# Kernel tuning notes

Measured on AMD Instinct MI355X. Metric: run time of the kernel, lower is better.

Reference implementation:

```python
import jax, jax.numpy as jnp
import numpy as np

N = 100000      # nodes
E = 1600000     # edges
G = 64          # graphs in batch
H = 128         # hidden (== num_features)
L = 4           # num_layers
C = 16          # num_classes
NCAND = 100000  # candidate edges
BN_EPS = 1e-5


def setup_inputs() -> dict:
    key = jax.random.key(0)
    ks = jax.random.split(key, 24)
    s = 0.05
    inp = {}
    inp["x"] = jax.random.normal(ks[0], (N, H), dtype=jnp.float32)
    inp["edge_index"] = jax.random.randint(ks[1], (2, E), 0, N)
    inp["batch"] = jnp.sort(jax.random.randint(ks[2], (N,), 0, G))
    inp["candidate_edges"] = jax.random.randint(ks[3], (2, NCAND), 0, N)
    # GIN conv params, stacked over L layers (all layers are H->H since num_features==hidden)
    inp["cW1"] = jax.random.normal(ks[4], (L, H, H), dtype=jnp.float32) * s
    inp["cb1"] = jnp.zeros((L, H), jnp.float32)
    inp["cW2"] = jax.random.normal(ks[5], (L, H, H), dtype=jnp.float32) * s
    inp["cb2"] = jnp.zeros((L, H), jnp.float32)
    inp["cgamma"] = jnp.ones((L, H), jnp.float32)
    inp["cbeta"] = jnp.zeros((L, H), jnp.float32)
    inp["ceps"] = jnp.zeros((L,), jnp.float32)  # train_eps=True, init 0
    # node classifier: L*H -> 2H -> H -> H -> C (dropout is identity in eval)
    inp["ncW1"] = jax.random.normal(ks[6], (L * H, 2 * H), dtype=jnp.float32) * s
    inp["ncb1"] = jnp.zeros((2 * H,), jnp.float32)
    inp["ncW2"] = jax.random.normal(ks[7], (2 * H, H), dtype=jnp.float32) * s
    inp["ncb2"] = jnp.zeros((H,), jnp.float32)
    inp["ncW3"] = jax.random.normal(ks[8], (H, H), dtype=jnp.float32) * s
    inp["ncb3"] = jnp.zeros((H,), jnp.float32)
    inp["ncW4"] = jax.random.normal(ks[9], (H, C), dtype=jnp.float32) * s
    inp["ncb4"] = jnp.zeros((C,), jnp.float32)
    # edge predictor: 2*L*H -> 2H -> H -> 1
    inp["epW1"] = jax.random.normal(ks[10], (2 * L * H, 2 * H), dtype=jnp.float32) * s
    inp["epb1"] = jnp.zeros((2 * H,), jnp.float32)
    inp["epW2"] = jax.random.normal(ks[11], (2 * H, H), dtype=jnp.float32) * s
    inp["epb2"] = jnp.zeros((H,), jnp.float32)
    inp["epW3"] = jax.random.normal(ks[12], (H, 1), dtype=jnp.float32) * s
    inp["epb3"] = jnp.zeros((1,), jnp.float32)
    return inp


def _forward(x, cW1, cb1, cW2, cb2, cgamma, cbeta, ceps,
             ncW1, ncb1, ncW2, ncb2, ncW3, ncb3, ncW4, ncb4,
             epW1, epb1, epW2, epb2, epW3, epb3,
             edge_index, batch, candidate_edges):
    src, dst = edge_index[0], edge_index[1]
    h = x
    xs = []
    for l in range(L):
        # GIN: (1+eps)*x_i + sum_{j->i} x_j  (scatter-add over destination nodes)
        agg = jax.ops.segment_sum(h[src], dst, num_segments=N)
        z = (1.0 + ceps[l]) * h + agg
        z = jax.nn.relu(z @ cW1[l] + cb1[l])
        z = jax.nn.relu(z @ cW2[l] + cb2[l])
        # BatchNorm1d (training-mode batch statistics, biased variance)
        mu = z.mean(axis=0)
        var = jnp.var(z, axis=0)
        h = (z - mu) * jax.lax.rsqrt(var + BN_EPS) * cgamma[l] + cbeta[l]
        xs.append(h)
    emb = jnp.concatenate(xs, axis=-1)  # [N, L*H]
    # global mean pool over graphs
    sums = jax.ops.segment_sum(emb, batch, num_segments=G)
    cnt = jax.ops.segment_sum(jnp.ones((N, 1), emb.dtype), batch, num_segments=G)
    gemb = sums / jnp.maximum(cnt, 1.0)  # [G, L*H]
    t = jax.nn.relu(gemb @ ncW1 + ncb1)
    t = jax.nn.relu(t @ ncW2 + ncb2)
    t = jax.nn.relu(t @ ncW3 + ncb3)
    class_output = jax.nn.log_softmax(t @ ncW4 + ncb4, axis=1)  # [G, C]
    # link prediction: gather node embeddings per candidate edge
    ef = jnp.concatenate([emb[candidate_edges[0]], emb[candidate_edges[1]]], axis=1)  # [NC, 2*L*H]
    u = jax.nn.relu(ef @ epW1 + epb1)
    u = jax.nn.relu(u @ epW2 + epb2)
    edge_scores = jax.nn.sigmoid((u @ epW3 + epb3).squeeze(-1))  # [NC]
    return class_output, edge_scores


def reference(x, cW1, cb1, cW2, cb2, cgamma, cbeta, ceps,
              ncW1, ncb1, ncW2, ncb2, ncW3, ncb3, ncW4, ncb4,
              epW1, epb1, epW2, epb2, epW3, epb3,
              edge_index, batch, candidate_edges):
    return _forward(x, cW1, cb1, cW2, cb2, cgamma, cbeta, ceps,
                    ncW1, ncb1, ncW2, ncb2, ncW3, ncb3, ncW4, ncb4,
                    epW1, epb1, epW2, epb2, epW3, epb3,
                    edge_index, batch, candidate_edges)
```

## Files before the change

kernel.cpp:

```cpp
#include <hip/hip_runtime.h>
#include <math.h>

#define NN 100000
#define EE 1600000
#define GG 64
#define HH 128
#define LL 4
#define CCLS 16
#define NC 100000
#define NB 49
#define LDK 40
#define LDA2 136
#define LDC 260

typedef __attribute__((ext_vector_type(8))) short bf16x8;
typedef __attribute__((ext_vector_type(4))) float f32x4;

__device__ __forceinline__ unsigned short f2bf(float x) {
  union { float f; unsigned int u; } v; v.f = x;
  unsigned int r = v.u + 0x7fffu + ((v.u >> 16) & 1u);
  return (unsigned short)(r >> 16);
}
__device__ __forceinline__ float bl(unsigned u) {
  union { unsigned u; float f; } v; v.u = u << 16; return v.f;
}
__device__ __forceinline__ float bh(unsigned u) {
  union { unsigned u; float f; } v; v.u = u & 0xffff0000u; return v.f;
}

__global__ void hist_kernel(const int* __restrict__ dst, int* __restrict__ cnt, int E) {
  int e = blockIdx.x * 256 + threadIdx.x;
  if (e < E) atomicAdd(&cnt[dst[e]], 1);
}

__global__ __launch_bounds__(256) void scan_p1(const int* __restrict__ cnt,
                                               int* __restrict__ bsum, int n) {
  __shared__ int red[256];
  int tid = threadIdx.x;
  int base = blockIdx.x * 1024 + tid * 4;
  int s = 0;
  if (base + 3 < n) {
    int4 v = *(const int4*)(cnt + base);
    s = v.x + v.y + v.z + v.w;
  } else {
    for (int i = 0; i < 4; ++i) if (base + i < n) s += cnt[base + i];
  }
  red[tid] = s;
  __syncthreads();
  for (int st = 128; st >= 1; st >>= 1) {
    if (tid < st) red[tid] += red[tid + st];
    __syncthreads();
  }
  if (tid == 0) bsum[blockIdx.x] = red[0];
}

__global__ void scan_p2(int* __restrict__ bsum, int* __restrict__ rowptr,
                        int* __restrict__ bcursor, int nb, int n) {
  __shared__ int buf[128];
  int tid = threadIdx.x;
  int v = (tid < nb) ? bsum[tid] : 0;
  buf[tid] = v;
  __syncthreads();
  for (int off = 1; off < 128; off <<= 1) {
    int t = (tid >= off) ? buf[tid - off] : 0;
    __syncthreads();
    buf[tid] += t;
    __syncthreads();
  }
  if (tid < nb) bsum[tid] = buf[tid] - v;
  if (tid == 127) rowptr[n] = buf[127];
  __syncthreads();
  if (tid < NB) bcursor[tid] = bsum[2 * tid];
}

__global__ __launch_bounds__(256) void scan_p3(const int* __restrict__ cnt,
                                               const int* __restrict__ bsum,
                                               int* __restrict__ rowptr,
                                               int* __restrict__ cursor, int n) {
  __shared__ int red[256];
  int tid = threadIdx.x;
  int base = blockIdx.x * 1024 + tid * 4;
  int v[4] = {0, 0, 0, 0};
  if (base + 3 < n) {
    int4 t = *(const int4*)(cnt + base);
    v[0] = t.x; v[1] = t.y; v[2] = t.z; v[3] = t.w;
  } else {
    for (int i = 0; i < 4; ++i) if (base + i < n) v[i] = cnt[base + i];
  }
  int s = v[0] + v[1] + v[2] + v[3];
  red[tid] = s;
  __syncthreads();
  for (int off = 1; off < 256; off <<= 1) {
    int t = (tid >= off) ? red[tid - off] : 0;
    __syncthreads();
    red[tid] += t;
    __syncthreads();
  }
  int run = bsum[blockIdx.x] + red[tid] - s;
  int4 o;
  o.x = run; o.y = run + v[0]; o.z = o.y + v[1]; o.w = o.z + v[2];
  if (base + 3 < n) {
    *(int4*)(rowptr + base) = o;
    *(int4*)(cursor + base) = o;
  } else {
    int oo[4] = {o.x, o.y, o.z, o.w};
    for (int i = 0; i < 4; ++i)
      if (base + i < n) { rowptr[base + i] = oo[i]; cursor[base + i] = oo[i]; }
  }
}

__global__ __launch_bounds__(256) void partition_kernel(const int* __restrict__ src,
                                                        const int* __restrict__ dst,
                                                        int* __restrict__ bcursor,
                                                        int2* __restrict__ pairs, int E) {
  __shared__ int sS[4096];
  __shared__ int sD[4096];
  __shared__ int hist[NB];
  __shared__ int base[NB];
  int tid = threadIdx.x;
  int base_e = blockIdx.x * 4096;
  int cnt = min(4096, E - base_e);
  if (tid < NB) hist[tid] = 0;
  for (int i = tid * 4; i < cnt; i += 1024) {
    if (i + 3 < cnt) {
      *(int4*)(sS + i) = *(const int4*)(src + base_e + i);
      *(int4*)(sD + i) = *(const int4*)(dst + base_e + i);
    } else {
      for (int k = i; k < cnt; ++k) { sS[k] = src[base_e + k]; sD[k] = dst[base_e + k]; }
    }
  }
  __syncthreads();
  for (int i = tid; i < cnt; i += 256) atomicAdd(&hist[sD[i] >> 11], 1);
  __syncthreads();
  if (tid < NB) {
    base[tid] = atomicAdd(&bcursor[tid], hist[tid]);
    hist[tid] = 0;
  }
  __syncthreads();
  for (int i = tid; i < cnt; i += 256) {
    int d = sD[i];
    int b = d >> 11;
    int off = atomicAdd(&hist[b], 1);
    pairs[base[b] + off] = make_int2(sS[i], d);
  }
}

__global__ __launch_bounds__(256) void scatter_csr(const int2* __restrict__ pairs,
                                                   const int* __restrict__ rowptr,
                                                   int* __restrict__ cursor,
                                                   int* __restrict__ csr_src) {
  int b = blockIdx.x % 56;
  int slice = blockIdx.x / 56;
  if (b >= NB) return;
  int start = rowptr[b * 2048];
  int endn = min((b + 1) * 2048, NN);
  int end = rowptr[endn];
  for (int i = start + slice * 256 + threadIdx.x; i < end; i += 8 * 256) {
    int2 p = pairs[i];
    int pos = atomicAdd(&cursor[p.y], 1);
    csr_src[pos] = p.x;
  }
}

__global__ void f2b4_kernel(const float* __restrict__ in, unsigned short* __restrict__ out, int n4) {
  int i = blockIdx.x * 256 + threadIdx.x;
  if (i >= n4) return;
  float4 v = ((const float4*)in)[i];
  unsigned short r[4] = {f2bf(v.x), f2bf(v.y), f2bf(v.z), f2bf(v.w)};
  *(uint2*)(out + (size_t)i * 4) = *(uint2*)r;
}

__global__ void conv_weights(const float* __restrict__ cW1, const float* __restrict__ cW2,
                             unsigned short* __restrict__ WT1, unsigned short* __restrict__ WT2,
                             const float* __restrict__ epW1, unsigned short* __restrict__ W1T,
                             const float* __restrict__ epW2, unsigned short* __restrict__ W2T) {
  int idx = blockIdx.x * 256 + threadIdx.x;
  if (idx < LL * 16384) {
    int l = idx >> 14, r = idx & 16383, k = r >> 7, n = r & 127;
    WT1[l * 16384 + n * 128 + k] = f2bf(cW1[idx]);
    WT2[l * 16384 + n * 128 + k] = f2bf(cW2[idx]);
  } else if (idx < LL * 16384 + 262144) {
    int j = idx - LL * 16384;
    int k = j >> 8, n = j & 255;
    W1T[(size_t)n * 1024 + k] = f2bf(epW1[j]);
  } else if (idx < LL * 16384 + 262144 + 32768) {
    int j = idx - LL * 16384 - 262144;
    int k = j >> 7, n = j & 127;
    W2T[(size_t)n * 256 + k] = f2bf(epW2[j]);
  }
}

__global__ void aggregate_bf16(const unsigned short* __restrict__ h16, int ld,
                               const int* __restrict__ rowptr,
                               const int* __restrict__ csr_src,
                               const float* __restrict__ ceps_l,
                               unsigned short* __restrict__ out, int n) {
  int wave = threadIdx.x >> 6;
  int lane = threadIdx.x & 63;
  int sub = lane >> 4;
  int li = lane & 15;
  int node = blockIdx.x * 16 + wave * 4 + sub;
  if (node >= n) return;
  int c8 = li * 8;
  float eps1 = 1.0f + *ceps_l;
  float acc[8] = {};
  int b = rowptr[node], e = rowptr[node + 1];
  int j = b;
  for (; j + 8 <= e; j += 8) {
    uint4 u[8];
#pragma unroll
    for (int t = 0; t < 8; ++t) {
      int s = csr_src[j + t];
      u[t] = *(const uint4*)(h16 + (size_t)s * ld + c8);
    }
#pragma unroll
    for (int t = 0; t < 8; ++t) {
      acc[0] += bl(u[t].x); acc[1] += bh(u[t].x);
      acc[2] += bl(u[t].y); acc[3] += bh(u[t].y);
      acc[4] += bl(u[t].z); acc[5] += bh(u[t].z);
      acc[6] += bl(u[t].w); acc[7] += bh(u[t].w);
    }
  }
  for (; j < e; ++j) {
    int s = csr_src[j];
    uint4 u = *(const uint4*)(h16 + (size_t)s * ld + c8);
    acc[0] += bl(u.x); acc[1] += bh(u.x);
    acc[2] += bl(u.y); acc[3] += bh(u.y);
    acc[4] += bl(u.z); acc[5] += bh(u.z);
    acc[6] += bl(u.w); acc[7] += bh(u.w);
  }
  uint4 hu = *(const uint4*)(h16 + (size_t)node * ld + c8);
  acc[0] = fmaf(eps1, bl(hu.x), acc[0]); acc[1] = fmaf(eps1, bh(hu.x), acc[1]);
  acc[2] = fmaf(eps1, bl(hu.y), acc[2]); acc[3] = fmaf(eps1, bh(hu.y), acc[3]);
  acc[4] = fmaf(eps1, bl(hu.z), acc[4]); acc[5] = fmaf(eps1, bh(hu.z), acc[5]);
  acc[6] = fmaf(eps1, bl(hu.w), acc[6]); acc[7] = fmaf(eps1, bh(hu.w), acc[7]);
  unsigned short o[8];
#pragma unroll
  for (int i = 0; i < 8; ++i) o[i] = f2bf(acc[i]);
  *(uint4*)(out + (size_t)node * 128 + c8) = *(uint4*)o;
}

__global__ __launch_bounds__(256) void trunk_fused(
    const unsigned short* __restrict__ A16,
    const unsigned short* __restrict__ W1T, const float* __restrict__ b1,
    const unsigned short* __restrict__ W2T, const float* __restrict__ b2,
    float* __restrict__ bnsum, float* __restrict__ bnsumsq,
    unsigned short* __restrict__ C16, int M) {
  __shared__ unsigned short As[128 * LDA2];
  __shared__ unsigned short Bs[128 * LDA2];
  const int tid = threadIdx.x;
  const int bm = blockIdx.x * 128;
  const int lane = tid & 63;
  const int wave = tid >> 6;
  const int wr = (wave >> 1) << 6;
  const int wc = (wave & 1) << 6;
  const int ar = tid >> 1;
  const int ah = (tid & 1) << 4;
  int gra = bm + ar; if (gra >= M) gra = M - 1;
  const unsigned short* Arow = A16 + (size_t)gra * 128;
  const unsigned short* B1row = W1T + (size_t)ar * 128;
  const int mrow = lane & 15;
  const int kq = (lane >> 4) << 3;

  {
    uint4 aR[8], bR[8];
#pragma unroll
    for (int i = 0; i < 4; ++i) {
      aR[2 * i]     = *(const uint4*)(Arow + (i << 5) + ah);
      aR[2 * i + 1] = *(const uint4*)(Arow + (i << 5) + ah + 8);
      bR[2 * i]     = *(const uint4*)(B1row + (i << 5) + ah);
      bR[2 * i + 1] = *(const uint4*)(B1row + (i << 5) + ah + 8);
    }
#pragma unroll
    for (int i = 0; i < 4; ++i) {
      *(uint4*)(As + ar * LDA2 + (i << 5) + ah)     = aR[2 * i];
      *(uint4*)(As + ar * LDA2 + (i << 5) + ah + 8) = aR[2 * i + 1];
      *(uint4*)(Bs + ar * LDA2 + (i << 5) + ah)     = bR[2 * i];
      *(uint4*)(Bs + ar * LDA2 + (i << 5) + ah + 8) = bR[2 * i + 1];
    }
  }
  f32x4 acc[4][4] = {};
  __syncthreads();
#pragma unroll
  for (int ks = 0; ks < 4; ++ks) {
    const int k0 = ks << 5;
    bf16x8 af[4], bfv[4];
#pragma unroll
    for (int t = 0; t < 4; ++t)
      af[t] = *(const bf16x8*)(As + (wr + t * 16 + mrow) * LDA2 + k0 + kq);
#pragma unroll
    for (int t = 0; t < 4; ++t)
      bfv[t] = *(const bf16x8*)(Bs + (wc + t * 16 + mrow) * LDA2 + k0 + kq);
#pragma unroll
    for (int mt = 0; mt < 4; ++mt)
#pragma unroll
      for (int nt = 0; nt < 4; ++nt)
        acc[mt][nt] = __builtin_amdgcn_mfma_f32_16x16x32_bf16(af[mt], bfv[nt], acc[mt][nt], 0, 0, 0);
  }
  uint4 w2[8];
  {
    const unsigned short* B2row = W2T + (size_t)ar * 128;
#pragma unroll
    for (int i = 0; i < 4; ++i) {
      w2[2 * i]     = *(const uint4*)(B2row + (i << 5) + ah);
      w2[2 * i + 1] = *(const uint4*)(B2row + (i << 5) + ah + 8);
    }
  }
  __syncthreads();
  const int crow = (lane >> 4) << 2;
  const int ccol = lane & 15;
#pragma unroll
  for (int nt = 0; nt < 4; ++nt) {
    int c = wc + nt * 16 + ccol;
    float bz = b1[c];
#pragma unroll
    for (int mt = 0; mt < 4; ++mt) {
      int rl = wr + mt * 16 + crow;
#pragma unroll
      for (int i = 0; i < 4; ++i)
        As[(rl + i) * LDA2 + c] = f2bf(fmaxf(acc[mt][nt][i] + bz, 0.f));
    }
  }
#pragma unroll
  for (int i = 0; i < 4; ++i) {
    *(uint4*)(Bs + ar * LDA2 + (i << 5) + ah)     = w2[2 * i];
    *(uint4*)(Bs + ar * LDA2 + (i << 5) + ah + 8) = w2[2 * i + 1];
  }
#pragma unroll
  for (int mt = 0; mt < 4; ++mt)
#pragma unroll
    for (int nt = 0; nt < 4; ++nt)
      acc[mt][nt] = (f32x4){0.f, 0.f, 0.f, 0.f};
  __syncthreads();
#pragma unroll
  for (int ks = 0; ks < 4; ++ks) {
    const int k0 = ks << 5;
    bf16x8 af[4], bfv[4];
#pragma unroll
    for (int t = 0; t < 4; ++t)
      af[t] = *(const bf16x8*)(As + (wr + t * 16 + mrow) * LDA2 + k0 + kq);
#pragma unroll
    for (int t = 0; t < 4; ++t)
      bfv[t] = *(const bf16x8*)(Bs + (wc + t * 16 + mrow) * LDA2 + k0 + kq);
#pragma unroll
    for (int mt = 0; mt < 4; ++mt)
#pragma unroll
      for (int nt = 0; nt < 4; ++nt)
        acc[mt][nt] = __builtin_amdgcn_mfma_f32_16x16x32_bf16(af[mt], bfv[nt], acc[mt][nt], 0, 0, 0);
  }
#pragma unroll
  for (int nt = 0; nt < 4; ++nt) {
    int c = wc + nt * 16 + ccol;
    float bz = b2[c];
    float s = 0.f, q = 0.f;
#pragma unroll
    for (int mt = 0; mt < 4; ++mt) {
      int rbase = bm + wr + mt * 16 + crow;
#pragma unroll
      for (int i = 0; i < 4; ++i) {
        int r = rbase + i;
        if (r < M) {
          float v = fmaxf(acc[mt][nt][i] + bz, 0.f);
          C16[(size_t)r * 128 + c] = f2bf(v);
          s += v; q += v * v;
        }
      }
    }
    s += __shfl_xor(s, 16, 64);
    s += __shfl_xor(s, 32, 64);
    q += __shfl_xor(q, 16, 64);
    q += __shfl_xor(q, 32, 64);
    if (lane < 16) {
      atomicAdd(&bnsum[c], s);
      atomicAdd(&bnsumsq[c], q);
    }
  }
}

__global__ __launch_bounds__(512, 4) void ep_fused(
    const unsigned short* __restrict__ emb16, const int* __restrict__ cand,
    const unsigned short* __restrict__ W1T ,
    const float* __restrict__ b1,
    const unsigned short* __restrict__ W2T ,
    const float* __restrict__ b2, const float* __restrict__ epW3,
    const float* __restrict__ epb3,
    float* __restrict__ out, int M) {
  __shared__ unsigned short smem[128 * LDC];
  __shared__ float sDot[128];
  unsigned short* const As0 = smem;
  unsigned short* const As1 = smem + 128 * LDK;
  unsigned short* const Bs0 = smem + 2 * 128 * LDK;
  unsigned short* const Bs1 = smem + 2 * 128 * LDK + 256 * LDK;
  const int tid = threadIdx.x;
  const int bm = blockIdx.x * 128;
  const int lane = tid & 63;
  const int wave = tid >> 6;
  const int wr = (wave >> 2) << 6;
  const int wc = (wave & 3) << 6;
  f32x4 acc[4][4] = {};
  const int ar = tid >> 2;
  const int ah = (tid & 3) << 3;
  int gra = bm + ar; if (gra >= M) gra = M - 1;
  const int node0 = cand[gra];
  const int node1 = cand[NC + gra];
  const int br = tid >> 1;
  const int bh8 = (tid & 1) << 4;
  const unsigned short* Brow = W1T + (size_t)br * 1024 + bh8;
  const unsigned short* Arow0 = emb16 + (size_t)node0 * 512 + ah;
  const unsigned short* Arow1 = emb16 + (size_t)node1 * 512 + ah - 512;
  const int mrow = lane & 15;
  const int kq = (lane >> 4) << 3;

  if (tid < 128) sDot[tid] = 0.f;

  auto ldA = [&](int k) -> uint4 {
    const unsigned short* p = (k < 16) ? Arow0 : Arow1;
    return *(const uint4*)(p + (k << 5));
  };
  auto ldB0v = [&](int k) -> uint4 { return *(const uint4*)(Brow + (k << 5)); };
  auto ldB1v = [&](int k) -> uint4 { return *(const uint4*)(Brow + (k << 5) + 8); };
  auto stTile = [&](unsigned short* Ab, unsigned short* Bb, uint4 a, uint4 x0, uint4 x1) {
    *(uint4*)(Ab + ar * LDK + ah) = a;
    *(uint4*)(Bb + br * LDK + bh8) = x0;
    *(uint4*)(Bb + br * LDK + bh8 + 8) = x1;
  };
  auto mma_step = [&](const unsigned short* A, const unsigned short* B) {
    bf16x8 af[4], bfv[4];
#pragma unroll
    for (int t = 0; t < 4; ++t)
      af[t] = *(const bf16x8*)(A + (wr + t * 16 + mrow) * LDK + kq);
#pragma unroll
    for (int t = 0; t < 4; ++t)
      bfv[t] = *(const bf16x8*)(B + (wc + t * 16 + mrow) * LDK + kq);
#pragma unroll
    for (int mt = 0; mt < 4; ++mt)
#pragma unroll
      for (int nt = 0; nt < 4; ++nt)
        acc[mt][nt] = __builtin_amdgcn_mfma_f32_16x16x32_bf16(af[mt], bfv[nt], acc[mt][nt], 0, 0, 0);
  };

  uint4 aA, aB, b0, b1v;
  {
    uint4 a0 = ldA(0), x0 = ldB0v(0), x1 = ldB1v(0);
    stTile(As0, Bs0, a0, x0, x1);
    aA = ldA(1); b0 = ldB0v(1); b1v = ldB1v(1);
    aB = ldA(2);
  }
  __syncthreads();
  for (int it = 0; it < 16; ++it) {
    const int s0 = 2 * it;
    stTile(As1, Bs1, aA, b0, b1v);
    if (s0 + 3 < 32) aA = ldA(s0 + 3);
    if (s0 + 2 < 32) { b0 = ldB0v(s0 + 2); b1v = ldB1v(s0 + 2); }
    mma_step(As0, Bs0);
    __syncthreads();
    const int s1 = s0 + 1;
    if (s1 < 31) {
      stTile(As0, Bs0, aB, b0, b1v);
      if (s1 + 3 < 32) aB = ldA(s1 + 3);
      if (s1 + 2 < 32) { b0 = ldB0v(s1 + 2); b1v = ldB1v(s1 + 2); }
    }
    mma_step(As1, Bs1);
    __syncthreads();
  }

  const int crow = (lane >> 4) << 2;
  const int ccol = lane & 15;
#pragma unroll
  for (int nt = 0; nt < 4; ++nt) {
    int c = wc + nt * 16 + ccol;
    float bz = b1[c];
#pragma unroll
    for (int mt = 0; mt < 4; ++mt) {
      int rl = wr + mt * 16 + crow;
#pragma unroll
      for (int i = 0; i < 4; ++i)
        smem[(rl + i) * LDC + c] = f2bf(fmaxf(acc[mt][nt][i] + bz, 0.f));
    }
  }
  __syncthreads();
  const int wr2 = (wave >> 1) << 5;
  const int wc2 = (wave & 1) << 6;
  f32x4 acc2[2][4] = {};
  for (int ks = 0; ks < 8; ++ks) {
    const int k0 = ks << 5;
    bf16x8 af[2], bfv[4];
#pragma unroll
    for (int t = 0; t < 2; ++t)
      af[t] = *(const bf16x8*)(smem + (wr2 + t * 16 + mrow) * LDC + k0 + kq);
#pragma unroll
    for (int t = 0; t < 4; ++t)
      bfv[t] = *(const bf16x8*)(W2T + (size_t)(wc2 + t * 16 + mrow) * 256 + k0 + kq);
#pragma unroll
    for (int mt = 0; mt < 2; ++mt)
#pragma unroll
      for (int nt = 0; nt < 4; ++nt)
        acc2[mt][nt] = __builtin_amdgcn_mfma_f32_16x16x32_bf16(af[mt], bfv[nt], acc2[mt][nt], 0, 0, 0);
  }
  float w3v[4], bz2[4];
#pragma unroll
  for (int nt = 0; nt < 4; ++nt) {
    int c = wc2 + nt * 16 + ccol;
    w3v[nt] = epW3[c];
    bz2[nt] = b2[c];
  }
#pragma unroll
  for (int mt = 0; mt < 2; ++mt) {
#pragma unroll
    for (int i = 0; i < 4; ++i) {
      int rl = wr2 + mt * 16 + crow + i;
      float p = 0.f;
#pragma unroll
      for (int nt = 0; nt < 4; ++nt)
        p = fmaf(fmaxf(acc2[mt][nt][i] + bz2[nt], 0.f), w3v[nt], p);
      atomicAdd(&sDot[rl], p);
    }
  }
  __syncthreads();
  if (tid < 128) {
    int r = bm + tid;
    if (r < M) out[r] = 1.f / (1.f + expf(-(sDot[tid] + epb3[0])));
  }
}

__global__ void bn_apply_bf16(const unsigned short* __restrict__ z,
                              const float* __restrict__ sum, const float* __restrict__ sumsq,
                              const float* __restrict__ gamma, const float* __restrict__ beta,
                              unsigned short* __restrict__ out, int n) {
  int idx = blockIdx.x * 256 + threadIdx.x;
  if (idx >= n * 16) return;
  int r = idx >> 4, c8 = (idx & 15) << 3;
  uint4 v = *(const uint4*)(z + (size_t)r * 128 + c8);
  float f[8] = {bl(v.x), bh(v.x), bl(v.y), bh(v.y), bl(v.z), bh(v.z), bl(v.w), bh(v.w)};
  const float inv_n = 1.0f / (float)NN;
  unsigned short o[8];
#pragma unroll
  for (int j = 0; j < 8; ++j) {
    int c = c8 + j;
    float mu = sum[c] * inv_n;
    float var = sumsq[c] * inv_n - mu * mu;
    float sc = rsqrtf(var + 1e-5f) * gamma[c];
    o[j] = f2bf((f[j] - mu) * sc + beta[c]);
  }
  *(uint4*)(out + (size_t)r * 512 + c8) = *(uint4*)o;
}

__global__ void bounds_kernel(const int* __restrict__ batch, int* __restrict__ gstart, int n) {
  int g = threadIdx.x;
  if (g > GG) return;
  int lo = 0, hi = n;
  while (lo < hi) {
    int mid = (lo + hi) >> 1;
    if (batch[mid] < g) lo = mid + 1; else hi = mid;
  }
  gstart[g] = lo;
}

__global__ __launch_bounds__(256) void pool_bf16(const unsigned short* __restrict__ emb16,
                                                 const int* __restrict__ gstart,
                                                 float* __restrict__ gsum) {
  int g = blockIdx.x;
  int chunk = blockIdx.y;
  int c2 = threadIdx.x * 2;
  int s = gstart[g], e = gstart[g + 1];
  int len = e - s;
  int per = (len + 7) >> 3;
  int r0 = s + chunk * per;
  int r1 = min(r0 + per, e);
  float ax = 0.f, ay = 0.f;
  for (int r = r0; r < r1; ++r) {
    unsigned u = *(const unsigned*)(emb16 + (size_t)r * 512 + c2);
    ax += bl(u); ay += bh(u);
  }
  if (r1 > r0) {
    atomicAdd(&gsum[g * 512 + c2], ax);
    atomicAdd(&gsum[g * 512 + c2 + 1], ay);
  }
}

__global__ __launch_bounds__(256) void nc_fused(
    const float* __restrict__ gsum, const int* __restrict__ gstart,
    const float* __restrict__ W1, const float* __restrict__ b1,
    const float* __restrict__ W2, const float* __restrict__ b2,
    const float* __restrict__ W3, const float* __restrict__ b3,
    const float* __restrict__ W4, const float* __restrict__ b4,
    float* __restrict__ out) {
  __shared__ float row[512];
  __shared__ float t1[256];
  __shared__ float t2[128];
  __shared__ float t3s[128];
  __shared__ float lg[16];
  int g = blockIdx.x;
  int tid = threadIdx.x;
  float inv = 1.0f / fmaxf((float)(gstart[g + 1] - gstart[g]), 1.0f);
  row[tid] = gsum[g * 512 + tid] * inv;
  row[tid + 256] = gsum[g * 512 + tid + 256] * inv;
  __syncthreads();
  {
    float acc = b1[tid];
#pragma unroll 8
    for (int k = 0; k < 512; ++k) acc = fmaf(row[k], W1[k * 256 + tid], acc);
    t1[tid] = fmaxf(acc, 0.f);
  }
  __syncthreads();
  if (tid < 128) {
    float acc = b2[tid];
#pragma unroll 8
    for (int k = 0; k < 256; ++k) acc = fmaf(t1[k], W2[k * 128 + tid], acc);
    t2[tid] = fmaxf(acc, 0.f);
  }
  __syncthreads();
  if (tid < 128) {
    float acc = b3[tid];
#pragma unroll 8
    for (int k = 0; k < 128; ++k) acc = fmaf(t2[k], W3[k * 128 + tid], acc);
    t3s[tid] = fmaxf(acc, 0.f);
  }
  __syncthreads();
  if (tid < 16) {
    float acc = b4[tid];
#pragma unroll 8
    for (int k = 0; k < 128; ++k) acc = fmaf(t3s[k], W4[k * 16 + tid], acc);
    lg[tid] = acc;
  }
  __syncthreads();
  if (tid < 16) {
    float v = lg[tid];
    float m = v;
    for (int j = 0; j < 16; ++j) m = fmaxf(m, lg[j]);
    float s = 0.f;
    for (int j = 0; j < 16; ++j) s += expf(lg[j] - m);
    out[g * 16 + tid] = v - m - logf(s);
  }
}

extern "C" void kernel_launch(void* const* d_in, const int* in_sizes, int n_in,
                              void* d_out, int out_size, void* d_ws, size_t ws_size,
                              hipStream_t stream) {
  const float* x = (const float*)d_in[0];
  const int* edge_index = (const int*)d_in[1];
  const int* batch = (const int*)d_in[2];
  const int* cand = (const int*)d_in[3];
  const float* cW1 = (const float*)d_in[4];
  const float* cb1 = (const float*)d_in[5];
  const float* cW2 = (const float*)d_in[6];
  const float* cb2 = (const float*)d_in[7];
  const float* cgamma = (const float*)d_in[8];
  const float* cbeta = (const float*)d_in[9];
  const float* ceps = (const float*)d_in[10];
  const float* ncW1 = (const float*)d_in[11];
  const float* ncb1 = (const float*)d_in[12];
  const float* ncW2 = (const float*)d_in[13];
  const float* ncb2 = (const float*)d_in[14];
  const float* ncW3 = (const float*)d_in[15];
  const float* ncb3 = (const float*)d_in[16];
  const float* ncW4 = (const float*)d_in[17];
  const float* ncb4 = (const float*)d_in[18];
  const float* epW1 = (const float*)d_in[19];
  const float* epb1 = (const float*)d_in[20];
  const float* epW2 = (const float*)d_in[21];
  const float* epb2 = (const float*)d_in[22];
  const float* epW3 = (const float*)d_in[23];
  const float* epb3 = (const float*)d_in[24];

  char* ws = (char*)d_ws;
  size_t off = 0;
  auto alloc = [&](size_t bytes) -> void* {
    off = (off + 255) & ~(size_t)255;
    void* p = ws + off;
    off += bytes;
    return p;
  };
  size_t zz_bytes = (size_t)NN * 4 + 512 * 4 + 512 * 4 + (size_t)GG * 512 * 4;
  char* zz = (char*)alloc(zz_bytes);
  int* cnt = (int*)zz;
  float* bnsum = (float*)(zz + (size_t)NN * 4);
  float* bnsumsq = bnsum + 512;
  float* gsum = bnsumsq + 512;
  int* rowptr = (int*)alloc((size_t)(NN + 1) * 4);
  int* cursor = (int*)alloc((size_t)NN * 4);
  int* csr_src = (int*)alloc((size_t)EE * 4);
  int2* pairs = (int2*)alloc((size_t)EE * 8);
  int* bsum = (int*)alloc(128 * 4);
  int* bcursor = (int*)alloc(64 * 4);
  unsigned short* x16 = (unsigned short*)alloc((size_t)NN * 128 * 2);
  unsigned short* g16a = (unsigned short*)alloc((size_t)NN * 128 * 2);
  unsigned short* emb16 = (unsigned short*)alloc((size_t)NN * 512 * 2);
  unsigned short* WT1 = (unsigned short*)alloc((size_t)LL * 16384 * 2);
  unsigned short* WT2 = (unsigned short*)alloc((size_t)LL * 16384 * 2);
  unsigned short* W1T = (unsigned short*)alloc((size_t)1024 * 256 * 2);
  unsigned short* W2T = (unsigned short*)alloc((size_t)256 * 128 * 2);
  int* gstart = (int*)alloc(65 * 4);

  const int* esrc = edge_index;
  const int* edst = edge_index + EE;
  const int nblk = (NN + 1023) / 1024;
  const int nech = (EE + 4095) / 4096;

  hipMemsetAsync(zz, 0, zz_bytes, stream);
  hist_kernel<<<(EE + 255) / 256, 256, 0, stream>>>(edst, cnt, EE);
  scan_p1<<<nblk, 256, 0, stream>>>(cnt, bsum, NN);
  scan_p2<<<1, 128, 0, stream>>>(bsum, rowptr, bcursor, nblk, NN);
  scan_p3<<<nblk, 256, 0, stream>>>(cnt, bsum, rowptr, cursor, NN);
  partition_kernel<<<nech, 256, 0, stream>>>(esrc, edst, bcursor, pairs, EE);
  scatter_csr<<<56 * 8, 256, 0, stream>>>(pairs, rowptr, cursor, csr_src);
  f2b4_kernel<<<(NN * 128 / 4 + 255) / 256, 256, 0, stream>>>(x, x16, NN * 128 / 4);
  conv_weights<<<(LL * 16384 + 262144 + 32768 + 255) / 256, 256, 0, stream>>>(
      cW1, cW2, WT1, WT2, epW1, W1T, epW2, W2T);

  for (int l = 0; l < LL; ++l) {
    const unsigned short* h16 = (l == 0) ? x16 : (emb16 + (size_t)(l - 1) * 128);
    int ld = (l == 0) ? 128 : 512;
    aggregate_bf16<<<(NN + 15) / 16, 256, 0, stream>>>(h16, ld, rowptr, csr_src, ceps + l, g16a, NN);
    trunk_fused<<<(NN + 127) / 128, 256, 0, stream>>>(
        g16a, WT1 + (size_t)l * 16384, cb1 + l * 128,
        WT2 + (size_t)l * 16384, cb2 + l * 128,
        bnsum + l * 128, bnsumsq + l * 128, g16a, NN);
    bn_apply_bf16<<<(NN * 16 + 255) / 256, 256, 0, stream>>>(
        g16a, bnsum + l * 128, bnsumsq + l * 128, cgamma + l * 128, cbeta + l * 128,
        emb16 + (size_t)l * 128, NN);
  }

  bounds_kernel<<<1, 128, 0, stream>>>(batch, gstart, NN);
  pool_bf16<<<dim3(GG, 8), 256, 0, stream>>>(emb16, gstart, gsum);
  nc_fused<<<GG, 256, 0, stream>>>(gsum, gstart, ncW1, ncb1, ncW2, ncb2, ncW3, ncb3,
                                   ncW4, ncb4, (float*)d_out);

  ep_fused<<<(NC + 127) / 128, 512, 0, stream>>>(
      emb16, cand, W1T, epb1, W2T, epb2, epW3, epb3,
      (float*)d_out + GG * CCLS, NC);
}
```

Before: 1.099 ms.

## Fold BatchNorm into next-layer aggregation and apply all layers' BN once

```diff
diff --git a/kernel.cpp b/kernel.cpp
--- a/kernel.cpp
+++ b/kernel.cpp
@@ -162,19 +162,21 @@
   }
 }
 
-__global__ void f2b4_kernel(const float* __restrict__ in, unsigned short* __restrict__ out, int n4) {
-  int i = blockIdx.x * 256 + threadIdx.x;
-  if (i >= n4) return;
-  float4 v = ((const float4*)in)[i];
-  unsigned short r[4] = {f2bf(v.x), f2bf(v.y), f2bf(v.z), f2bf(v.w)};
-  *(uint2*)(out + (size_t)i * 4) = *(uint2*)r;
-}
-
-__global__ void conv_weights(const float* __restrict__ cW1, const float* __restrict__ cW2,
-                             unsigned short* __restrict__ WT1, unsigned short* __restrict__ WT2,
-                             const float* __restrict__ epW1, unsigned short* __restrict__ W1T,
-                             const float* __restrict__ epW2, unsigned short* __restrict__ W2T) {
-  int idx = blockIdx.x * 256 + threadIdx.x;
+#define NF2B (NN * HH / 4)
+#define NCVW (LL * 16384 + 262144 + 32768)
+__global__ void convert_all(const float* __restrict__ x, unsigned short* __restrict__ x16,
+                            const float* __restrict__ cW1, const float* __restrict__ cW2,
+                            unsigned short* __restrict__ WT1, unsigned short* __restrict__ WT2,
+                            const float* __restrict__ epW1, unsigned short* __restrict__ W1T,
+                            const float* __restrict__ epW2, unsigned short* __restrict__ W2T) {
+  int gi = blockIdx.x * 256 + threadIdx.x;
+  if (gi < NF2B) {
+    float4 v = ((const float4*)x)[gi];
+    unsigned short r[4] = {f2bf(v.x), f2bf(v.y), f2bf(v.z), f2bf(v.w)};
+    *(uint2*)(x16 + (size_t)gi * 4) = *(uint2*)r;
+    return;
+  }
+  int idx = gi - NF2B;
   if (idx < LL * 16384) {
     int l = idx >> 14, r = idx & 16383, k = r >> 7, n = r & 127;
     WT1[l * 16384 + n * 128 + k] = f2bf(cW1[idx]);
@@ -183,7 +185,7 @@
     int j = idx - LL * 16384;
     int k = j >> 8, n = j & 255;
     W1T[(size_t)n * 1024 + k] = f2bf(epW1[j]);
-  } else if (idx < LL * 16384 + 262144 + 32768) {
+  } else if (idx < NCVW) {
     int j = idx - LL * 16384 - 262144;
     int k = j >> 7, n = j & 127;
     W2T[(size_t)n * 256 + k] = f2bf(epW2[j]);
@@ -194,6 +196,10 @@
                                const int* __restrict__ rowptr,
                                const int* __restrict__ csr_src,
                                const float* __restrict__ ceps_l,
+                               const float* __restrict__ bnsum_prev,
+                               const float* __restrict__ bnsumsq_prev,
+                               const float* __restrict__ gamma_prev,
+                               const float* __restrict__ beta_prev,
                                unsigned short* __restrict__ out, int n) {
   int wave = threadIdx.x >> 6;
   int lane = threadIdx.x & 63;
@@ -203,6 +209,22 @@
   if (node >= n) return;
   int c8 = li * 8;
   float eps1 = 1.0f + *ceps_l;
+  float sc[8], off[8];
+  if (bnsum_prev) {
+    const float inv_n = 1.0f / (float)NN;
+#pragma unroll
+    for (int k = 0; k < 8; ++k) {
+      int c = c8 + k;
+      float mu = bnsum_prev[c] * inv_n;
+      float var = bnsumsq_prev[c] * inv_n - mu * mu;
+      float s = rsqrtf(var + 1e-5f) * gamma_prev[c];
+      sc[k] = s;
+      off[k] = beta_prev[c] - s * mu;
+    }
+  } else {
+#pragma unroll
+    for (int k = 0; k < 8; ++k) { sc[k] = 1.f; off[k] = 0.f; }
+  }
   float acc[8] = {};
   int b = rowptr[node], e = rowptr[node + 1];
   int j = b;
@@ -234,9 +256,10 @@
   acc[2] = fmaf(eps1, bl(hu.y), acc[2]); acc[3] = fmaf(eps1, bh(hu.y), acc[3]);
   acc[4] = fmaf(eps1, bl(hu.z), acc[4]); acc[5] = fmaf(eps1, bh(hu.z), acc[5]);
   acc[6] = fmaf(eps1, bl(hu.w), acc[6]); acc[7] = fmaf(eps1, bh(hu.w), acc[7]);
+  float degw = (float)(e - b) + eps1;
   unsigned short o[8];
 #pragma unroll
-  for (int i = 0; i < 8; ++i) o[i] = f2bf(acc[i]);
+  for (int i = 0; i < 8; ++i) o[i] = f2bf(fmaf(sc[i], acc[i], degw * off[i]));
   *(uint4*)(out + (size_t)node * 128 + c8) = *(uint4*)o;
 }
 
@@ -245,7 +268,7 @@
     const unsigned short* __restrict__ W1T, const float* __restrict__ b1,
     const unsigned short* __restrict__ W2T, const float* __restrict__ b2,
     float* __restrict__ bnsum, float* __restrict__ bnsumsq,
-    unsigned short* __restrict__ C16, int M) {
+    unsigned short* __restrict__ C16 , int M) {
   __shared__ unsigned short As[128 * LDA2];
   __shared__ unsigned short Bs[128 * LDA2];
   const int tid = threadIdx.x;
@@ -361,7 +384,7 @@
         int r = rbase + i;
         if (r < M) {
           float v = fmaxf(acc[mt][nt][i] + bz, 0.f);
-          C16[(size_t)r * 128 + c] = f2bf(v);
+          C16[(size_t)r * 512 + c] = f2bf(v);
           s += v; q += v * v;
         }
       }
@@ -375,6 +398,27 @@
       atomicAdd(&bnsumsq[c], q);
     }
   }
+}
+
+__global__ void bn_all(unsigned short* __restrict__ z ,
+                       const float* __restrict__ sum, const float* __restrict__ sumsq,
+                       const float* __restrict__ gamma, const float* __restrict__ beta) {
+  int idx = blockIdx.x * 256 + threadIdx.x;
+  if (idx >= NN * 64) return;
+  int r = idx >> 6, c8 = (idx & 63) << 3;
+  uint4 v = *(const uint4*)(z + (size_t)r * 512 + c8);
+  float f[8] = {bl(v.x), bh(v.x), bl(v.y), bh(v.y), bl(v.z), bh(v.z), bl(v.w), bh(v.w)};
+  const float inv_n = 1.0f / (float)NN;
+  unsigned short o[8];
+#pragma unroll
+  for (int j = 0; j < 8; ++j) {
+    int c = c8 + j;
+    float mu = sum[c] * inv_n;
+    float var = sumsq[c] * inv_n - mu * mu;
+    float scv = rsqrtf(var + 1e-5f) * gamma[c];
+    o[j] = f2bf((f[j] - mu) * scv + beta[c]);
+  }
+  *(uint4*)(z + (size_t)r * 512 + c8) = *(uint4*)o;
 }
 
 __global__ __launch_bounds__(512, 4) void ep_fused(
@@ -386,7 +430,8 @@
     const float* __restrict__ epb3,
     float* __restrict__ out, int M) {
   __shared__ unsigned short smem[128 * LDC];
-  __shared__ float sDot[128];
+  __shared__ float sDotA[128];
+  __shared__ float sDotB[128];
   unsigned short* const As0 = smem;
   unsigned short* const As1 = smem + 128 * LDK;
   unsigned short* const Bs0 = smem + 2 * 128 * LDK;
@@ -411,8 +456,6 @@
   const int mrow = lane & 15;
   const int kq = (lane >> 4) << 3;
 
-  if (tid < 128) sDot[tid] = 0.f;
-
   auto ldA = [&](int k) -> uint4 {
     const unsigned short* p = (k < 16) ? Arow0 : Arow1;
     return *(const uint4*)(p + (k << 5));
@@ -504,6 +547,7 @@
     w3v[nt] = epW3[c];
     bz2[nt] = b2[c];
   }
+  float* sBank = (wave & 1) ? sDotB : sDotA;
 #pragma unroll
   for (int mt = 0; mt < 2; ++mt) {
 #pragma unroll
@@ -513,56 +557,38 @@
 #pragma unroll
       for (int nt = 0; nt < 4; ++nt)
         p = fmaf(fmaxf(acc2[mt][nt][i] + bz2[nt], 0.f), w3v[nt], p);
-      atomicAdd(&sDot[rl], p);
+      p += __shfl_xor(p, 1, 64);
+      p += __shfl_xor(p, 2, 64);
+      p += __shfl_xor(p, 4, 64);
+      p += __shfl_xor(p, 8, 64);
+      if ((lane & 15) == 0) sBank[rl] = p;
     }
   }
   __syncthreads();
   if (tid < 128) {
     int r = bm + tid;
-    if (r < M) out[r] = 1.f / (1.f + expf(-(sDot[tid] + epb3[0])));
-  }
-}
-
-__global__ void bn_apply_bf16(const unsigned short* __restrict__ z,
-                              const float* __restrict__ sum, const float* __restrict__ sumsq,
-                              const float* __restrict__ gamma, const float* __restrict__ beta,
-                              unsigned short* __restrict__ out, int n) {
-  int idx = blockIdx.x * 256 + threadIdx.x;
-  if (idx >= n * 16) return;
-  int r = idx >> 4, c8 = (idx & 15) << 3;
-  uint4 v = *(const uint4*)(z + (size_t)r * 128 + c8);
-  float f[8] = {bl(v.x), bh(v.x), bl(v.y), bh(v.y), bl(v.z), bh(v.z), bl(v.w), bh(v.w)};
-  const float inv_n = 1.0f / (float)NN;
-  unsigned short o[8];
-#pragma unroll
-  for (int j = 0; j < 8; ++j) {
-    int c = c8 + j;
-    float mu = sum[c] * inv_n;
-    float var = sumsq[c] * inv_n - mu * mu;
-    float sc = rsqrtf(var + 1e-5f) * gamma[c];
-    o[j] = f2bf((f[j] - mu) * sc + beta[c]);
-  }
-  *(uint4*)(out + (size_t)r * 512 + c8) = *(uint4*)o;
-}
-
-__global__ void bounds_kernel(const int* __restrict__ batch, int* __restrict__ gstart, int n) {
-  int g = threadIdx.x;
-  if (g > GG) return;
-  int lo = 0, hi = n;
-  while (lo < hi) {
-    int mid = (lo + hi) >> 1;
-    if (batch[mid] < g) lo = mid + 1; else hi = mid;
-  }
-  gstart[g] = lo;
+    if (r < M) out[r] = 1.f / (1.f + expf(-(sDotA[tid] + sDotB[tid] + epb3[0])));
+  }
 }
 
 __global__ __launch_bounds__(256) void pool_bf16(const unsigned short* __restrict__ emb16,
-                                                 const int* __restrict__ gstart,
+                                                 const int* __restrict__ batch,
                                                  float* __restrict__ gsum) {
+  __shared__ int se[2];
   int g = blockIdx.x;
   int chunk = blockIdx.y;
+  if (threadIdx.x < 2) {
+    int x = g + (int)threadIdx.x;
+    int lo = 0, hi = NN;
+    while (lo < hi) {
+      int mid = (lo + hi) >> 1;
+      if (batch[mid] < x) lo = mid + 1; else hi = mid;
+    }
+    se[threadIdx.x] = lo;
+  }
+  __syncthreads();
+  int s = se[0], e = se[1];
   int c2 = threadIdx.x * 2;
-  int s = gstart[g], e = gstart[g + 1];
   int len = e - s;
   int per = (len + 7) >> 3;
   int r0 = s + chunk * per;
@@ -579,7 +605,7 @@
 }
 
 __global__ __launch_bounds__(256) void nc_fused(
-    const float* __restrict__ gsum, const int* __restrict__ gstart,
+    const float* __restrict__ gsum, const int* __restrict__ batch,
     const float* __restrict__ W1, const float* __restrict__ b1,
     const float* __restrict__ W2, const float* __restrict__ b2,
     const float* __restrict__ W3, const float* __restrict__ b3,
@@ -590,9 +616,20 @@
   __shared__ float t2[128];
   __shared__ float t3s[128];
   __shared__ float lg[16];
+  __shared__ int se[2];
   int g = blockIdx.x;
   int tid = threadIdx.x;
-  float inv = 1.0f / fmaxf((float)(gstart[g + 1] - gstart[g]), 1.0f);
+  if (tid < 2) {
+    int x = g + tid;
+    int lo = 0, hi = NN;
+    while (lo < hi) {
+      int mid = (lo + hi) >> 1;
+      if (batch[mid] < x) lo = mid + 1; else hi = mid;
+    }
+    se[tid] = lo;
+  }
+  __syncthreads();
+  float inv = 1.0f / fmaxf((float)(se[1] - se[0]), 1.0f);
   row[tid] = gsum[g * 512 + tid] * inv;
   row[tid + 256] = gsum[g * 512 + tid + 256] * inv;
   __syncthreads();
@@ -690,7 +727,6 @@
   unsigned short* WT2 = (unsigned short*)alloc((size_t)LL * 16384 * 2);
   unsigned short* W1T = (unsigned short*)alloc((size_t)1024 * 256 * 2);
   unsigned short* W2T = (unsigned short*)alloc((size_t)256 * 128 * 2);
-  int* gstart = (int*)alloc(65 * 4);
 
   const int* esrc = edge_index;
   const int* edst = edge_index + EE;
@@ -704,26 +740,28 @@
   scan_p3<<<nblk, 256, 0, stream>>>(cnt, bsum, rowptr, cursor, NN);
   partition_kernel<<<nech, 256, 0, stream>>>(esrc, edst, bcursor, pairs, EE);
   scatter_csr<<<56 * 8, 256, 0, stream>>>(pairs, rowptr, cursor, csr_src);
-  f2b4_kernel<<<(NN * 128 / 4 + 255) / 256, 256, 0, stream>>>(x, x16, NN * 128 / 4);
-  conv_weights<<<(LL * 16384 + 262144 + 32768 + 255) / 256, 256, 0, stream>>>(
-      cW1, cW2, WT1, WT2, epW1, W1T, epW2, W2T);
+  convert_all<<<(NF2B + NCVW + 255) / 256, 256, 0, stream>>>(
+      x, x16, cW1, cW2, WT1, WT2, epW1, W1T, epW2, W2T);
 
   for (int l = 0; l < LL; ++l) {
     const unsigned short* h16 = (l == 0) ? x16 : (emb16 + (size_t)(l - 1) * 128);
     int ld = (l == 0) ? 128 : 512;
-    aggregate_bf16<<<(NN + 15) / 16, 256, 0, stream>>>(h16, ld, rowptr, csr_src, ceps + l, g16a, NN);
+    aggregate_bf16<<<(NN + 15) / 16, 256, 0, stream>>>(
+        h16, ld, rowptr, csr_src, ceps + l,
+        (l == 0) ? nullptr : bnsum + (l - 1) * 128,
+        (l == 0) ? nullptr : bnsumsq + (l - 1) * 128,
+        (l == 0) ? nullptr : cgamma + (l - 1) * 128,
+        (l == 0) ? nullptr : cbeta + (l - 1) * 128,
+        g16a, NN);
     trunk_fused<<<(NN + 127) / 128, 256, 0, stream>>>(
         g16a, WT1 + (size_t)l * 16384, cb1 + l * 128,
         WT2 + (size_t)l * 16384, cb2 + l * 128,
-        bnsum + l * 128, bnsumsq + l * 128, g16a, NN);
-    bn_apply_bf16<<<(NN * 16 + 255) / 256, 256, 0, stream>>>(
-        g16a, bnsum + l * 128, bnsumsq + l * 128, cgamma + l * 128, cbeta + l * 128,
-        emb16 + (size_t)l * 128, NN);
-  }
-
-  bounds_kernel<<<1, 128, 0, stream>>>(batch, gstart, NN);
-  pool_bf16<<<dim3(GG, 8), 256, 0, stream>>>(emb16, gstart, gsum);
-  nc_fused<<<GG, 256, 0, stream>>>(gsum, gstart, ncW1, ncb1, ncW2, ncb2, ncW3, ncb3,
+        bnsum + l * 128, bnsumsq + l * 128, emb16 + (size_t)l * 128, NN);
+  }
+  bn_all<<<(NN * 64 + 255) / 256, 256, 0, stream>>>(emb16, bnsum, bnsumsq, cgamma, cbeta);
+
+  pool_bf16<<<dim3(GG, 8), 256, 0, stream>>>(emb16, batch, gsum);
+  nc_fused<<<GG, 256, 0, stream>>>(gsum, batch, ncW1, ncb1, ncW2, ncb2, ncW3, ncb3,
                                    ncW4, ncb4, (float*)d_out);
 
   ep_fused<<<(NC + 127) / 128, 512, 0, stream>>>(
```

New measurement: 1.094 ms. Within noise of the previous version (-0.5%).
